# Kernel optimization log

Measured on AMD Instinct MI355X. Metric: run time of the kernel, lower is better.

The kernel has to match this reference:

```python
import jax, jax.numpy as jnp
import numpy as np

N_NODES = 10000
N_EDGES = 160000
NEG_SLOPE = 0.2
DIMS = [(128, 1024), (1024, 512), (512, 128)]
NUM_CLASSES = 64


def _glorot(k, shape):
    lim = np.sqrt(6.0 / (shape[0] + shape[1])).astype(np.float32)
    return jax.random.uniform(k, shape, jnp.float32, -lim, lim)


def setup_inputs() -> dict:
    key = jax.random.key(0)
    ks = iter(jax.random.split(key, 32))
    inp = {
        'x': jax.random.normal(next(ks), (N_NODES, DIMS[0][0]), jnp.float32),
        'edge_index': jax.random.randint(next(ks), (2, N_EDGES), 0, N_NODES, jnp.int64),
    }
    for i, (fin, fout) in enumerate(DIMS, start=1):
        inp[f'Wl{i}'] = _glorot(next(ks), (fin, fout))
        inp[f'bl{i}'] = jnp.zeros((fout,), jnp.float32)
        inp[f'Wr{i}'] = _glorot(next(ks), (fin, fout))
        inp[f'br{i}'] = jnp.zeros((fout,), jnp.float32)
        inp[f'att{i}'] = _glorot(next(ks), (1, fout))[0]
        inp[f'b{i}'] = jnp.zeros((fout,), jnp.float32)
    inp['Wc'] = _glorot(next(ks), (DIMS[-1][1], NUM_CLASSES))
    inp['bc'] = jnp.zeros((NUM_CLASSES,), jnp.float32)
    return inp


def _gatv2(x, src, dst, Wl, bl, Wr, br, att, b):
    # PyG GATv2Conv, heads=1, add_self_loops=True (self-loops appended by caller)
    n = x.shape[0]
    xl = x @ Wl + bl          # source-side transform [N, F]
    xr = x @ Wr + br          # target-side transform [N, F]
    m = xl[src] + xr[dst]     # [E, F] per-edge message
    e = jax.nn.leaky_relu(m, NEG_SLOPE) @ att  # [E] attention logits
    # segment softmax over incoming edges of each dst node
    emax = jax.ops.segment_max(e, dst, num_segments=n)
    ez = jnp.exp(e - emax[dst])
    denom = jax.ops.segment_sum(ez, dst, num_segments=n)
    alpha = ez / denom[dst]
    out = jax.ops.segment_sum(alpha[:, None] * xl[src], dst, num_segments=n)
    return out + b


def reference(x, edge_index, Wl1, bl1, Wr1, br1, att1, b1,
              Wl2, bl2, Wr2, br2, att2, b2,
              Wl3, bl3, Wr3, br3, att3, b3, Wc, bc):
    n = x.shape[0]
    loops = jnp.arange(n, dtype=edge_index.dtype)
    src = jnp.concatenate([edge_index[0], loops])
    dst = jnp.concatenate([edge_index[1], loops])
    h = jax.nn.relu(_gatv2(x, src, dst, Wl1, bl1, Wr1, br1, att1, b1))
    h = jax.nn.relu(_gatv2(h, src, dst, Wl2, bl2, Wr2, br2, att2, b2))
    h = jax.nn.relu(_gatv2(h, src, dst, Wl3, bl3, Wr3, br3, att3, b3))
    return h @ Wc + bc
```

## Files before the change

kernel.cpp:

```cpp
#include <hip/hip_runtime.h>


typedef __attribute__((ext_vector_type(8))) short bf16x8;
typedef __attribute__((ext_vector_type(4))) float f32x4;

__device__ __forceinline__ unsigned short bf16rn(float x) {
    union { float f; unsigned int u; } v; v.f = x;
    unsigned int r = v.u + 0x7FFF + ((v.u >> 16) & 1);
    return (unsigned short)(r >> 16);
}
__device__ __forceinline__ float bf16tof(unsigned short h) {
    union { unsigned int u; float f; } v; v.u = ((unsigned int)h) << 16;
    return v.f;
}

typedef __attribute__((address_space(1))) const void* gptr_t;
typedef __attribute__((address_space(3))) void* sptr_t;
__device__ __forceinline__ void gload_lds16(const void* g, void* l) {
    __builtin_amdgcn_global_load_lds((gptr_t)g, (sptr_t)l, 16, 0, 0);
}


__global__ __launch_bounds__(256) void splitT_kernel(
    const float* __restrict__ W, unsigned short* __restrict__ Th,
    unsigned short* __restrict__ Tl, int K, int F)
{
    __shared__ float tile[32][33];
    const int tx = threadIdx.x & 31, ty = threadIdx.x >> 5;
    const int k0 = blockIdx.x * 32, f0 = blockIdx.y * 32;
#pragma unroll
    for (int i = 0; i < 32; i += 8)
        tile[ty + i][tx] = W[(size_t)(k0 + ty + i) * F + f0 + tx];
    __syncthreads();
#pragma unroll
    for (int i = 0; i < 32; i += 8) {
        int f = f0 + ty + i, k = k0 + tx;
        float v = tile[tx][ty + i];
        unsigned short h = bf16rn(v);
        Th[(size_t)f * K + k] = h;
        Tl[(size_t)f * K + k] = bf16rn(v - bf16tof(h));
    }
}

__global__ void split_kernel(const float* __restrict__ X,
                             unsigned short* __restrict__ Hi,
                             unsigned short* __restrict__ Lo, int n4)
{
    int i = blockIdx.x * blockDim.x + threadIdx.x;
    if (i >= n4) return;
    float4 v = ((const float4*)X)[i];
    ushort4 h, l;
    h.x = bf16rn(v.x); l.x = bf16rn(v.x - bf16tof(h.x));
    h.y = bf16rn(v.y); l.y = bf16rn(v.y - bf16tof(h.y));
    h.z = bf16rn(v.z); l.z = bf16rn(v.z - bf16tof(h.z));
    h.w = bf16rn(v.w); l.w = bf16rn(v.w - bf16tof(h.w));
    ((ushort4*)Hi)[i] = h;
    ((ushort4*)Lo)[i] = l;
}


template<int BM, int BN>
__global__ __launch_bounds__(256) void gemm_mfma_t(
    const unsigned short* __restrict__ Ahi, const unsigned short* __restrict__ Alo,
    int M, int K,
    const unsigned short* __restrict__ WThA, const unsigned short* __restrict__ WTlA,
    const unsigned short* __restrict__ WThB, const unsigned short* __restrict__ WTlB,
    const float* __restrict__ biasA, const float* __restrict__ biasB,
    float* __restrict__ CA, float* __restrict__ CB, int F)
{
    constexpr int GA = BM / 16, GB = BN / 16;
    constexpr int NJ = (2 * GA + 2 * GB) / 4;
    constexpr int WM = BM / 2, WN = BN / 2;
    constexpr int MI = WM / 16, NI = WN / 16;

    __shared__ unsigned short Ash[BM * 32];
    __shared__ unsigned short Asl[BM * 32];
    __shared__ unsigned short Bsh[BN * 32];
    __shared__ unsigned short Bsl[BN * 32];

    const int t = threadIdx.x;
    const int lane = t & 63, wave = t >> 6;
    const int nyh = (int)gridDim.y >> 1;
    const int half = ((int)blockIdx.y >= nyh) ? 1 : 0;
    const int colBase = ((int)blockIdx.y - half * nyh) * BN;
    const unsigned short* WTh = half ? WThB : WThA;
    const unsigned short* WTl = half ? WTlB : WTlA;
    const float* bias = half ? biasB : biasA;
    float* C = half ? CB : CA;
    const int rowBase = (int)blockIdx.x * BM;

    const int wr = wave >> 1, wc = wave & 1;
    const int fr = lane & 15, g = lane >> 4;

    const int srow = lane >> 2;
    const int schunk = ((lane & 3) ^ ((lane >> 3) & 3)) * 8;

    const unsigned short* gsrc[NJ];
    unsigned short* ldst[NJ];
#pragma unroll
    for (int j = 0; j < NJ; ++j) {
        const int grp = wave + 4 * j;
        if (grp < GA) {
            int ga = rowBase + grp * 16 + srow; if (ga > M - 1) ga = M - 1;
            gsrc[j] = Ahi + (size_t)ga * K + schunk;
            ldst[j] = &Ash[grp * 512];
        } else if (grp < 2 * GA) {
            const int r16 = grp - GA;
            int ga = rowBase + r16 * 16 + srow; if (ga > M - 1) ga = M - 1;
            gsrc[j] = Alo + (size_t)ga * K + schunk;
            ldst[j] = &Asl[r16 * 512];
        } else if (grp < 2 * GA + GB) {
            const int r16 = grp - 2 * GA;
            const int gb = colBase + r16 * 16 + srow;
            gsrc[j] = WTh + (size_t)gb * K + schunk;
            ldst[j] = &Bsh[r16 * 512];
        } else {
            const int r16 = grp - 2 * GA - GB;
            const int gb = colBase + r16 * 16 + srow;
            gsrc[j] = WTl + (size_t)gb * K + schunk;
            ldst[j] = &Bsl[r16 * 512];
        }
    }

    f32x4 acc[MI][NI];
#pragma unroll
    for (int i = 0; i < MI; ++i)
#pragma unroll
        for (int j = 0; j < NI; ++j) acc[i][j] = (f32x4)(0.f);

    const int fragoff = (fr * 4 + (g ^ ((fr >> 1) & 3))) * 8;

    for (int k0 = 0; k0 < K; k0 += 32) {
#pragma unroll
        for (int j = 0; j < NJ; ++j) gload_lds16(gsrc[j] + k0, ldst[j]);
        __syncthreads();

        bf16x8 ah[MI], al[MI], bh[NI], bl[NI];
#pragma unroll
        for (int mi = 0; mi < MI; ++mi) {
            ah[mi] = *(const bf16x8*)&Ash[(wr * MI + mi) * 512 + fragoff];
            al[mi] = *(const bf16x8*)&Asl[(wr * MI + mi) * 512 + fragoff];
        }
#pragma unroll
        for (int ni = 0; ni < NI; ++ni) {
            bh[ni] = *(const bf16x8*)&Bsh[(wc * NI + ni) * 512 + fragoff];
            bl[ni] = *(const bf16x8*)&Bsl[(wc * NI + ni) * 512 + fragoff];
        }
#pragma unroll
        for (int mi = 0; mi < MI; ++mi)
#pragma unroll
            for (int ni = 0; ni < NI; ++ni) {
                acc[mi][ni] = __builtin_amdgcn_mfma_f32_16x16x32_bf16(ah[mi], bh[ni], acc[mi][ni], 0, 0, 0);
                acc[mi][ni] = __builtin_amdgcn_mfma_f32_16x16x32_bf16(ah[mi], bl[ni], acc[mi][ni], 0, 0, 0);
                acc[mi][ni] = __builtin_amdgcn_mfma_f32_16x16x32_bf16(al[mi], bh[ni], acc[mi][ni], 0, 0, 0);
            }
        __syncthreads();
    }

#pragma unroll
    for (int mi = 0; mi < MI; ++mi) {
        const int row0 = rowBase + wr * WM + mi * 16 + g * 4;
#pragma unroll
        for (int ni = 0; ni < NI; ++ni) {
            const int col = colBase + wc * WN + ni * 16 + fr;
            const float b = bias[col];
#pragma unroll
            for (int r = 0; r < 4; ++r) {
                const int row = row0 + r;
                if (row < M) C[(size_t)row * F + col] = acc[mi][ni][r] + b;
            }
        }
    }
}


static constexpr int BMc = 64, BNc = 64, BKc = 16;

__global__ __launch_bounds__(256) void gemm_bias_kernel(
    const float* __restrict__ A, const float* __restrict__ W,
    const float* __restrict__ bias, float* __restrict__ C,
    int M, int K, int F)
{
    __shared__ float As[BKc][BMc];
    __shared__ float Bs[BKc][BNc];
    const int t = threadIdx.x;
    const int bm = blockIdx.x, bn = blockIdx.y;
    const int ty = t >> 4, tx = t & 15;
    const int rowBase = bm * BMc;
    const int colBase = bn * BNc;
    const int aRow = t & 63;
    const int aK = (t >> 6) << 2;
    const int gARow = min(rowBase + aRow, M - 1);
    const int bRow = t >> 4;
    const int bCol = (t & 15) << 2;

    float acc[4][4] = {{0.f, 0.f, 0.f, 0.f}};

    for (int k0 = 0; k0 < K; k0 += BKc) {
        float4 av = *(const float4*)&A[(size_t)gARow * K + k0 + aK];
        float4 bv = *(const float4*)&W[(size_t)(k0 + bRow) * F + colBase + bCol];
        As[aK + 0][aRow] = av.x;
        As[aK + 1][aRow] = av.y;
        As[aK + 2][aRow] = av.z;
        As[aK + 3][aRow] = av.w;
        *(float4*)&Bs[bRow][bCol] = bv;
        __syncthreads();
#pragma unroll
        for (int kk = 0; kk < BKc; ++kk) {
            float4 a4 = *(const float4*)&As[kk][ty << 2];
            float4 b4 = *(const float4*)&Bs[kk][tx << 2];
            float ar[4] = {a4.x, a4.y, a4.z, a4.w};
            float br_[4] = {b4.x, b4.y, b4.z, b4.w};
#pragma unroll
            for (int i = 0; i < 4; ++i)
#pragma unroll
                for (int j = 0; j < 4; ++j)
                    acc[i][j] += ar[i] * br_[j];
        }
        __syncthreads();
    }

    float4 bias4 = *(const float4*)&bias[colBase + (tx << 2)];
    float bb[4] = {bias4.x, bias4.y, bias4.z, bias4.w};
#pragma unroll
    for (int i = 0; i < 4; ++i) {
        int r = rowBase + (ty << 2) + i;
        if (r < M) {
            float4 o;
            o.x = acc[i][0] + bb[0];
            o.y = acc[i][1] + bb[1];
            o.z = acc[i][2] + bb[2];
            o.w = acc[i][3] + bb[3];
            *(float4*)&C[(size_t)r * F + colBase + (tx << 2)] = o;
        }
    }
}


__global__ void zero_ints_kernel(int* __restrict__ p, int n)
{
    int i = blockIdx.x * blockDim.x + threadIdx.x;
    if (i < n) p[i] = 0;
}

__device__ inline void edge_src_dst(const int* __restrict__ ei, int edge,
                                    int E_orig, int& src, int& dst)
{
    if (edge < E_orig) {
        src = ei[edge];
        dst = ei[E_orig + edge];
    } else {
        src = dst = edge - E_orig;
    }
}

__global__ void count_kernel(const int* __restrict__ ei, int E_orig, int E_tot,
                             int* __restrict__ counts)
{
    int e = blockIdx.x * blockDim.x + threadIdx.x;
    if (e >= E_tot) return;
    int src, dst;
    edge_src_dst(ei, e, E_orig, src, dst);
    atomicAdd(&counts[dst], 1);
}

__global__ __launch_bounds__(256) void scan_kernel(const int* __restrict__ counts, int n,
                                                   int* __restrict__ offsets,
                                                   int* __restrict__ cursor)
{
    __shared__ int part[256];
    const int t = threadIdx.x;
    const int chunk = (n + 255) >> 8;
    const int begin = t * chunk;
    const int end = min(begin + chunk, n);
    int s = 0;
    for (int i = begin; i < end; ++i) s += counts[i];
    part[t] = s;
    __syncthreads();
    for (int off = 1; off < 256; off <<= 1) {
        int v = (t >= off) ? part[t - off] : 0;
        __syncthreads();
        part[t] += v;
        __syncthreads();
    }
    int run = (t == 0) ? 0 : part[t - 1];
    for (int i = begin; i < end; ++i) {
        offsets[i] = run;
        cursor[i] = run;
        run += counts[i];
    }
    if (t == 255) offsets[n] = part[255];
}

__global__ void fill_kernel(const int* __restrict__ ei, int E_orig, int E_tot,
                            int* __restrict__ cursor, int* __restrict__ csr_src)
{
    int e = blockIdx.x * blockDim.x + threadIdx.x;
    if (e >= E_tot) return;
    int src, dst;
    edge_src_dst(ei, e, E_orig, src, dst);
    int pos = atomicAdd(&cursor[dst], 1);
    csr_src[pos] = src;
}


template<int F, bool SPLIT, int B>
__global__ __launch_bounds__(256) void fused_gat_wave_kernel(
    const float* __restrict__ xl, const float* __restrict__ xr,
    const float* __restrict__ att, const int* __restrict__ offsets,
    const int* __restrict__ csr_src, const float* __restrict__ bias,
    float* __restrict__ out_f32,
    unsigned short* __restrict__ out_hi, unsigned short* __restrict__ out_lo,
    int N)
{
    constexpr int VEC = F / 64;
    constexpr int CW = (VEC >= 4) ? 4 : VEC;
    constexpr int NC = VEC / CW;
    const int wave = threadIdx.x >> 6, lane = threadIdx.x & 63;
    const int n = blockIdx.x * 4 + wave;
    if (n >= N) return;
    const int start = offsets[n], end = offsets[n + 1];

    float xr_r[VEC], att_r[VEC], acc[VEC];
#pragma unroll
    for (int j = 0; j < NC; ++j)
#pragma unroll
        for (int c = 0; c < CW; ++c) {
            const int f = j * 64 * CW + lane * CW + c;
            xr_r[j * CW + c] = xr[(size_t)n * F + f];
            att_r[j * CW + c] = att[f];
            acc[j * CW + c] = 0.f;
        }

    float m = -1e30f, d = 0.f;

    for (int i = start; i < end; i += B) {
        int srcs[B];
#pragma unroll
        for (int b = 0; b < B; ++b) srcs[b] = csr_src[min(i + b, end - 1)];

        float r[B][VEC];
#pragma unroll
        for (int b = 0; b < B; ++b) {
            const float* row = xl + (size_t)srcs[b] * F;
#pragma unroll
            for (int j = 0; j < NC; ++j) {
                if constexpr (CW == 4) {
                    float4 v = *(const float4*)&row[j * 256 + lane * 4];
                    r[b][j * 4 + 0] = v.x; r[b][j * 4 + 1] = v.y;
                    r[b][j * 4 + 2] = v.z; r[b][j * 4 + 3] = v.w;
                } else {
                    float2 v = *(const float2*)&row[lane * 2];
                    r[b][0] = v.x; r[b][1] = v.y;
                }
            }
        }

        float p[B];
#pragma unroll
        for (int b = 0; b < B; ++b) {
            float pp = 0.f;
#pragma unroll
            for (int v = 0; v < VEC; ++v) {
                float mm = r[b][v] + xr_r[v];
                mm = fmaxf(mm, 0.2f * mm);
                pp += mm * att_r[v];
            }
            p[b] = pp;
        }

#pragma unroll
        for (int off = 32; off; off >>= 1)
#pragma unroll
            for (int b = 0; b < B; ++b) p[b] += __shfl_xor(p[b], off);

#pragma unroll
        for (int b = 0; b < B; ++b)
            if (i + b >= end) p[b] = -1e30f;

        float bmax = p[0];
#pragma unroll
        for (int b = 1; b < B; ++b) bmax = fmaxf(bmax, p[b]);
        const float nm = fmaxf(m, bmax);
        const float scale = __expf(m - nm);
        float w[B], wsum = 0.f;
#pragma unroll
        for (int b = 0; b < B; ++b) { w[b] = __expf(p[b] - nm); wsum += w[b]; }
        d = d * scale + wsum;
#pragma unroll
        for (int v = 0; v < VEC; ++v) {
            float a = acc[v] * scale;
#pragma unroll
            for (int b = 0; b < B; ++b) a += w[b] * r[b][v];
            acc[v] = a;
        }
        m = nm;
    }

    const float inv = 1.0f / d;
#pragma unroll
    for (int j = 0; j < NC; ++j) {
        float o[CW];
#pragma unroll
        for (int c = 0; c < CW; ++c) {
            const int f = j * 64 * CW + lane * CW + c;
            o[c] = fmaxf(acc[j * CW + c] * inv + bias[f], 0.f);
        }
        const size_t base = (size_t)n * F + j * 64 * CW + lane * CW;
        if constexpr (SPLIT) {
            if constexpr (CW == 4) {
                ushort4 h, l;
                h.x = bf16rn(o[0]); l.x = bf16rn(o[0] - bf16tof(h.x));
                h.y = bf16rn(o[1]); l.y = bf16rn(o[1] - bf16tof(h.y));
                h.z = bf16rn(o[2]); l.z = bf16rn(o[2] - bf16tof(h.z));
                h.w = bf16rn(o[3]); l.w = bf16rn(o[3] - bf16tof(h.w));
                *(ushort4*)&out_hi[base] = h;
                *(ushort4*)&out_lo[base] = l;
            } else {
                ushort2 h, l;
                h.x = bf16rn(o[0]); l.x = bf16rn(o[0] - bf16tof(h.x));
                h.y = bf16rn(o[1]); l.y = bf16rn(o[1] - bf16tof(h.y));
                *(ushort2*)&out_hi[base] = h;
                *(ushort2*)&out_lo[base] = l;
            }
        } else {
            if constexpr (CW == 4) {
                float4 v = {o[0], o[1], o[2], o[3]};
                *(float4*)&out_f32[base] = v;
            } else {
                float2 v = {o[0], o[1]};
                *(float2*)&out_f32[base] = v;
            }
        }
    }
}


extern "C" void kernel_launch(void* const* d_in, const int* in_sizes, int n_in,
                              void* d_out, int out_size, void* d_ws, size_t ws_size,
                              hipStream_t stream)
{
    const float* x   = (const float*)d_in[0];
    const int*   ei  = (const int*)d_in[1];
    const float* Wl1 = (const float*)d_in[2];
    const float* bl1 = (const float*)d_in[3];
    const float* Wr1 = (const float*)d_in[4];
    const float* br1 = (const float*)d_in[5];
    const float* at1 = (const float*)d_in[6];
    const float* b1  = (const float*)d_in[7];
    const float* Wl2 = (const float*)d_in[8];
    const float* bl2 = (const float*)d_in[9];
    const float* Wr2 = (const float*)d_in[10];
    const float* br2 = (const float*)d_in[11];
    const float* at2 = (const float*)d_in[12];
    const float* b2  = (const float*)d_in[13];
    const float* Wl3 = (const float*)d_in[14];
    const float* bl3 = (const float*)d_in[15];
    const float* Wr3 = (const float*)d_in[16];
    const float* br3 = (const float*)d_in[17];
    const float* at3 = (const float*)d_in[18];
    const float* b3  = (const float*)d_in[19];
    const float* Wc  = (const float*)d_in[20];
    const float* bc  = (const float*)d_in[21];

    const int N = in_sizes[0] / 128;
    const int E_orig = in_sizes[1] / 2;
    const int E_tot = E_orig + N;

    size_t off = 0;
    auto alloc = [&](size_t bytes) -> char* {
        char* p = (char*)d_ws + off;
        off += (bytes + 255) & ~(size_t)255;
        return p;
    };
    float* bufA = (float*)alloc((size_t)N * 1024 * 4);
    float* bufB = (float*)alloc((size_t)N * 1024 * 4);
    unsigned short* S_hi = (unsigned short*)alloc((size_t)N * 1024 * 2);
    unsigned short* S_lo = (unsigned short*)alloc((size_t)N * 1024 * 2);
    unsigned short* WThl = (unsigned short*)alloc((size_t)524288 * 2);
    unsigned short* WTll = (unsigned short*)alloc((size_t)524288 * 2);
    unsigned short* WThr = (unsigned short*)alloc((size_t)524288 * 2);
    unsigned short* WTlr = (unsigned short*)alloc((size_t)524288 * 2);
    int* counts  = (int*)alloc((size_t)N * 4);
    int* offsets = (int*)alloc((size_t)(N + 1) * 4);
    int* cursor  = (int*)alloc((size_t)N * 4);
    int* csr_src = (int*)alloc((size_t)E_tot * 4);
    (void)ws_size; (void)n_in; (void)out_size;

    const int eb = (E_tot + 255) / 256;
    const int mb128 = (N + 127) / 128;
    const int mb64  = (N + 63) / 64;
    const int nb4 = (N + 3) / 4;

    zero_ints_kernel<<<(N + 255) / 256, 256, 0, stream>>>(counts, N);
    count_kernel<<<eb, 256, 0, stream>>>(ei, E_orig, E_tot, counts);
    scan_kernel<<<1, 256, 0, stream>>>(counts, N, offsets, cursor);
    fill_kernel<<<eb, 256, 0, stream>>>(ei, E_orig, E_tot, cursor, csr_src);

    split_kernel<<<(N * 128 / 4 + 255) / 256, 256, 0, stream>>>(x, S_hi, S_lo, N * 128 / 4);

    splitT_kernel<<<dim3(128 / 32, 1024 / 32), 256, 0, stream>>>(Wl1, WThl, WTll, 128, 1024);
    splitT_kernel<<<dim3(128 / 32, 1024 / 32), 256, 0, stream>>>(Wr1, WThr, WTlr, 128, 1024);
    gemm_mfma_t<128, 128><<<dim3(mb128, 16), 256, 0, stream>>>(
        S_hi, S_lo, N, 128, WThl, WTll, WThr, WTlr, bl1, br1, bufA, bufB, 1024);
    fused_gat_wave_kernel<1024, true, 4><<<nb4, 256, 0, stream>>>(
        bufA, bufB, at1, offsets, csr_src, b1, nullptr, S_hi, S_lo, N);

    splitT_kernel<<<dim3(1024 / 32, 512 / 32), 256, 0, stream>>>(Wl2, WThl, WTll, 1024, 512);
    splitT_kernel<<<dim3(1024 / 32, 512 / 32), 256, 0, stream>>>(Wr2, WThr, WTlr, 1024, 512);
    gemm_mfma_t<128, 64><<<dim3(mb128, 16), 256, 0, stream>>>(
        S_hi, S_lo, N, 1024, WThl, WTll, WThr, WTlr, bl2, br2, bufA, bufB, 512);
    fused_gat_wave_kernel<512, true, 4><<<nb4, 256, 0, stream>>>(
        bufA, bufB, at2, offsets, csr_src, b2, nullptr, S_hi, S_lo, N);

    splitT_kernel<<<dim3(512 / 32, 128 / 32), 256, 0, stream>>>(Wl3, WThl, WTll, 512, 128);
    splitT_kernel<<<dim3(512 / 32, 128 / 32), 256, 0, stream>>>(Wr3, WThr, WTlr, 512, 128);
    gemm_mfma_t<64, 64><<<dim3(mb64, 4), 256, 0, stream>>>(
        S_hi, S_lo, N, 512, WThl, WTll, WThr, WTlr, bl3, br3, bufA, bufB, 128);
    fused_gat_wave_kernel<128, false, 8><<<nb4, 256, 0, stream>>>(
        bufA, bufB, at3, offsets, csr_src, b3, bufB, nullptr, nullptr, N);

    gemm_bias_kernel<<<dim3((N + BMc - 1) / BMc, 64 / BNc), 256, 0, stream>>>(
        bufB, Wc, bc, (float*)d_out, N, 128, 64);
}
```

Measured before the change: 454.1 us.

## Double-buffer GEMM LDS tiles, remap blocks across XCDs, enlarge layer-2 tile

The split-bf16 MFMA GEMM now keeps two LDS stages and issues the next K-tile's global-to-LDS loads before computing on the current one. The goal is to overlap memory latency with MFMA work. The launch grid becomes 1D and is remapped so consecutive tiles land on the same XCD, which should improve L2 reuse of shared A rows. Layer 2 also switches from 128x64 to 128x128 tiles. The cost is double LDS use, which may lower occupancy, and the loop keeps a single barrier per iteration, which could be racy if the async LDS loads are not fenced properly.

```diff
diff --git a/kernel.cpp b/kernel.cpp
--- a/kernel.cpp
+++ b/kernel.cpp
@@ -66,28 +66,38 @@
     const unsigned short* __restrict__ WThA, const unsigned short* __restrict__ WTlA,
     const unsigned short* __restrict__ WThB, const unsigned short* __restrict__ WTlB,
     const float* __restrict__ biasA, const float* __restrict__ biasB,
-    float* __restrict__ CA, float* __restrict__ CB, int F)
+    float* __restrict__ CA, float* __restrict__ CB, int F, int nby)
 {
     constexpr int GA = BM / 16, GB = BN / 16;
     constexpr int NJ = (2 * GA + 2 * GB) / 4;
     constexpr int WM = BM / 2, WN = BN / 2;
     constexpr int MI = WM / 16, NI = WN / 16;
-
-    __shared__ unsigned short Ash[BM * 32];
-    __shared__ unsigned short Asl[BM * 32];
-    __shared__ unsigned short Bsh[BN * 32];
-    __shared__ unsigned short Bsl[BN * 32];
+    constexpr int ASZ = BM * 32, BSZ = BN * 32;
+
+    __shared__ unsigned short Ash[2 * ASZ];
+    __shared__ unsigned short Asl[2 * ASZ];
+    __shared__ unsigned short Bsh[2 * BSZ];
+    __shared__ unsigned short Bsl[2 * BSZ];
 
     const int t = threadIdx.x;
     const int lane = t & 63, wave = t >> 6;
-    const int nyh = (int)gridDim.y >> 1;
-    const int half = ((int)blockIdx.y >= nyh) ? 1 : 0;
-    const int colBase = ((int)blockIdx.y - half * nyh) * BN;
+
+    const int nwg = (int)gridDim.x;
+    const int bid = (int)blockIdx.x;
+    const int q = nwg >> 3, r = nwg & 7;
+    const int xcd = bid & 7, slot = bid >> 3;
+    const int gidx = (xcd < r) ? (xcd * (q + 1) + slot)
+                               : (r * (q + 1) + (xcd - r) * q + slot);
+    const int bx = gidx / nby, byi = gidx % nby;
+
+    const int nyh = nby >> 1;
+    const int half = (byi >= nyh) ? 1 : 0;
+    const int colBase = (byi - half * nyh) * BN;
     const unsigned short* WTh = half ? WThB : WThA;
     const unsigned short* WTl = half ? WTlB : WTlA;
     const float* bias = half ? biasB : biasA;
     float* C = half ? CB : CA;
-    const int rowBase = (int)blockIdx.x * BM;
+    const int rowBase = bx * BM;
 
     const int wr = wave >> 1, wc = wave & 1;
     const int fr = lane & 15, g = lane >> 4;
@@ -122,6 +132,15 @@
         }
     }
 
+    auto stage = [&](int dbuf, int koff) {
+#pragma unroll
+        for (int j = 0; j < NJ; ++j) {
+            const int grp = wave + 4 * j;
+            const int pl = (grp < 2 * GA) ? ASZ : BSZ;
+            gload_lds16(gsrc[j] + koff, ldst[j] + dbuf * pl);
+        }
+    };
+
     f32x4 acc[MI][NI];
 #pragma unroll
     for (int i = 0; i < MI; ++i)
@@ -130,21 +149,24 @@
 
     const int fragoff = (fr * 4 + (g ^ ((fr >> 1) & 3))) * 8;
 
-    for (int k0 = 0; k0 < K; k0 += 32) {
-#pragma unroll
-        for (int j = 0; j < NJ; ++j) gload_lds16(gsrc[j] + k0, ldst[j]);
-        __syncthreads();
+    stage(0, 0);
+    __syncthreads();
+
+    const int nt = K >> 5;
+    for (int tt = 0; tt < nt; ++tt) {
+        const int cur = tt & 1;
+        if (tt + 1 < nt) stage(cur ^ 1, (tt + 1) * 32);
 
         bf16x8 ah[MI], al[MI], bh[NI], bl[NI];
 #pragma unroll
         for (int mi = 0; mi < MI; ++mi) {
-            ah[mi] = *(const bf16x8*)&Ash[(wr * MI + mi) * 512 + fragoff];
-            al[mi] = *(const bf16x8*)&Asl[(wr * MI + mi) * 512 + fragoff];
+            ah[mi] = *(const bf16x8*)&Ash[cur * ASZ + (wr * MI + mi) * 512 + fragoff];
+            al[mi] = *(const bf16x8*)&Asl[cur * ASZ + (wr * MI + mi) * 512 + fragoff];
         }
 #pragma unroll
         for (int ni = 0; ni < NI; ++ni) {
-            bh[ni] = *(const bf16x8*)&Bsh[(wc * NI + ni) * 512 + fragoff];
-            bl[ni] = *(const bf16x8*)&Bsl[(wc * NI + ni) * 512 + fragoff];
+            bh[ni] = *(const bf16x8*)&Bsh[cur * BSZ + (wc * NI + ni) * 512 + fragoff];
+            bl[ni] = *(const bf16x8*)&Bsl[cur * BSZ + (wc * NI + ni) * 512 + fragoff];
         }
 #pragma unroll
         for (int mi = 0; mi < MI; ++mi)
@@ -165,9 +187,9 @@
             const int col = colBase + wc * WN + ni * 16 + fr;
             const float b = bias[col];
 #pragma unroll
-            for (int r = 0; r < 4; ++r) {
-                const int row = row0 + r;
-                if (row < M) C[(size_t)row * F + col] = acc[mi][ni][r] + b;
+            for (int rr = 0; rr < 4; ++rr) {
+                const int row = row0 + rr;
+                if (row < M) C[(size_t)row * F + col] = acc[mi][ni][rr] + b;
             }
         }
     }
@@ -501,22 +523,22 @@
 
     splitT_kernel<<<dim3(128 / 32, 1024 / 32), 256, 0, stream>>>(Wl1, WThl, WTll, 128, 1024);
     splitT_kernel<<<dim3(128 / 32, 1024 / 32), 256, 0, stream>>>(Wr1, WThr, WTlr, 128, 1024);
-    gemm_mfma_t<128, 128><<<dim3(mb128, 16), 256, 0, stream>>>(
-        S_hi, S_lo, N, 128, WThl, WTll, WThr, WTlr, bl1, br1, bufA, bufB, 1024);
+    gemm_mfma_t<128, 128><<<mb128 * 16, 256, 0, stream>>>(
+        S_hi, S_lo, N, 128, WThl, WTll, WThr, WTlr, bl1, br1, bufA, bufB, 1024, 16);
     fused_gat_wave_kernel<1024, true, 4><<<nb4, 256, 0, stream>>>(
         bufA, bufB, at1, offsets, csr_src, b1, nullptr, S_hi, S_lo, N);
 
     splitT_kernel<<<dim3(1024 / 32, 512 / 32), 256, 0, stream>>>(Wl2, WThl, WTll, 1024, 512);
     splitT_kernel<<<dim3(1024 / 32, 512 / 32), 256, 0, stream>>>(Wr2, WThr, WTlr, 1024, 512);
-    gemm_mfma_t<128, 64><<<dim3(mb128, 16), 256, 0, stream>>>(
-        S_hi, S_lo, N, 1024, WThl, WTll, WThr, WTlr, bl2, br2, bufA, bufB, 512);
+    gemm_mfma_t<128, 128><<<mb128 * 8, 256, 0, stream>>>(
+        S_hi, S_lo, N, 1024, WThl, WTll, WThr, WTlr, bl2, br2, bufA, bufB, 512, 8);
     fused_gat_wave_kernel<512, true, 4><<<nb4, 256, 0, stream>>>(
         bufA, bufB, at2, offsets, csr_src, b2, nullptr, S_hi, S_lo, N);
 
     splitT_kernel<<<dim3(512 / 32, 128 / 32), 256, 0, stream>>>(Wl3, WThl, WTll, 512, 128);
     splitT_kernel<<<dim3(512 / 32, 128 / 32), 256, 0, stream>>>(Wr3, WThr, WTlr, 512, 128);
-    gemm_mfma_t<64, 64><<<dim3(mb64, 4), 256, 0, stream>>>(
-        S_hi, S_lo, N, 512, WThl, WTll, WThr, WTlr, bl3, br3, bufA, bufB, 128);
+    gemm_mfma_t<64, 64><<<mb64 * 4, 256, 0, stream>>>(
+        S_hi, S_lo, N, 512, WThl, WTll, WThr, WTlr, bl3, br3, bufA, bufB, 128, 4);
     fused_gat_wave_kernel<128, false, 8><<<nb4, 256, 0, stream>>>(
         bufA, bufB, at3, offsets, csr_src, b3, bufB, nullptr, nullptr, N);
 
```

After: 395.8 us. 1.15x faster.
